# Optimization experiments

Hardware: AMD Instinct MI355X
Metric: run time of the kernel (lower is better)

Reference implementation:

```python
import math
import jax, jax.numpy as jnp
import numpy as np

T = 4096          # sequence length
H = 2048          # hidden_size
I = 8192          # intermediate_size = 4*H
LAYER_ID = 1
N_LAYERS = 24
EPS = 1e-5        # layer_norm_epsilon


def setup_inputs() -> dict:
    key = jax.random.key(0)
    ks = jax.random.split(key, 8)
    s = 1.0 / math.sqrt(H)
    si = 1.0 / math.sqrt(I)
    r0 = LAYER_ID / (N_LAYERS - 1)          # ratio_0_to_1
    r1 = 1.0 - LAYER_ID / N_LAYERS          # ratio_1_to_almost_0
    h = jnp.arange(H, dtype=jnp.float32)
    x = h / H
    time_decay = -5.0 + 8.0 * (h / (H - 1)) ** (0.7 + 1.3 * r0)
    zigzag = 0.5 * ((jnp.arange(1, H + 1) % 3).astype(jnp.float32) - 1.0)
    time_first = jnp.full((H,), math.log(0.3), jnp.float32) + zigzag
    tm_key = x ** r1
    tm_value = tm_key + 0.3 * r0
    tm_recep = x ** (0.5 * r1)
    return {
        "hidden": jax.random.normal(ks[0], (T, H), jnp.float32),
        "att_sx": jnp.zeros((H,), jnp.float32),
        "att_aa": jnp.zeros((H,), jnp.float32),
        "att_bb": jnp.zeros((H,), jnp.float32),
        "att_pp": jnp.full((H,), -1e30, jnp.float32),  # log-space -inf init
        "ffd_sx": jnp.zeros((H,), jnp.float32),
        "ln1_scale": jnp.ones((H,), jnp.float32),
        "ln1_bias": jnp.zeros((H,), jnp.float32),
        "ln2_scale": jnp.ones((H,), jnp.float32),
        "ln2_bias": jnp.zeros((H,), jnp.float32),
        "time_decay": time_decay.astype(jnp.float32),
        "time_first": time_first,
        "tm_key": tm_key.astype(jnp.float32),
        "tm_value": tm_value.astype(jnp.float32),
        "tm_recep": tm_recep.astype(jnp.float32),
        "Wk": jax.random.normal(ks[1], (H, H), jnp.float32) * s,
        "Wv": jax.random.normal(ks[2], (H, H), jnp.float32) * s,
        "Wr": jax.random.normal(ks[3], (H, H), jnp.float32) * s,
        "Wo": jax.random.normal(ks[4], (H, H), jnp.float32) * s,
        "ffn_tm_key": (x ** r1).astype(jnp.float32),
        "ffn_tm_recep": (x ** (0.5 * r1)).astype(jnp.float32),
        "Wfk": jax.random.normal(ks[5], (H, I), jnp.float32) * s,
        "Wfr": jax.random.normal(ks[6], (H, H), jnp.float32) * s,
        "Wfv": jax.random.normal(ks[7], (I, H), jnp.float32) * si,
    }


def _ln(x, scale, bias):
    mu = jnp.mean(x, axis=-1, keepdims=True)
    var = jnp.mean(jnp.square(x - mu), axis=-1, keepdims=True)
    return (x - mu) * jax.lax.rsqrt(var + EPS) * scale + bias


def _block(hidden, att_sx, att_aa, att_bb, att_pp, ffd_sx,
           ln1_scale, ln1_bias, ln2_scale, ln2_bias,
           time_decay, time_first, tm_key, tm_value, tm_recep,
           Wk, Wv, Wr, Wo, ffn_tm_key, ffn_tm_recep, Wfk, Wfr, Wfv):
    # ---- attention (WKV) sub-block ----
    x1 = _ln(hidden, ln1_scale, ln1_bias)               # [T,H]
    c_x = jnp.concatenate((att_sx[None, :], x1[:-1, :]), axis=0)  # token shift
    kx = x1 * tm_key + c_x * (1.0 - tm_key)
    vx = x1 * tm_value + c_x * (1.0 - tm_value)
    rx = x1 * tm_recep + c_x * (1.0 - tm_recep)
    r = jax.nn.sigmoid(rx @ Wr)                         # [T,H]
    k = kx @ Wk
    v = vx @ Wv
    w_decay = -jnp.exp(time_decay)                      # [H]

    def step(carry, kv):
        aa, bb, pp = carry
        kk, vv = kv
        ww = time_first + kk
        p = jnp.maximum(pp, ww)
        e1 = jnp.exp(pp - p)
        e2 = jnp.exp(ww - p)
        out_t = (e1 * aa + e2 * vv) / (e1 * bb + e2)
        ww2 = w_decay + pp
        p2 = jnp.maximum(ww2, kk)
        e1b = jnp.exp(ww2 - p2)
        e2b = jnp.exp(kk - p2)
        return (e1b * aa + e2b * vv, e1b * bb + e2b, p2), out_t

    (aa, bb, pp), cx = jax.lax.scan(step, (att_aa, att_bb, att_pp), (k, v))
    attention = x1 + (r * cx) @ Wo                      # inner residual (as in source)
    hidden2 = hidden + attention

    # ---- feed-forward (channel-mix) sub-block ----
    x2 = _ln(hidden2, ln2_scale, ln2_bias)
    sx2 = jnp.concatenate((ffd_sx[None, :], x2[:-1, :]), axis=0)
    fk = x2 * ffn_tm_key + sx2 * (1.0 - ffn_tm_key)
    fr = x2 * ffn_tm_recep + sx2 * (1.0 - ffn_tm_recep)
    rr = jax.nn.sigmoid(fr @ Wfr)
    kk2 = jnp.square(jax.nn.relu(fk @ Wfk))             # [T,I]
    ffn = rr * (kk2 @ Wfv)
    out = hidden2 + ffn
    return out, x1[-1, :], aa, bb, pp, x2[-1, :]


def reference(hidden, att_sx, att_aa, att_bb, att_pp, ffd_sx,
              ln1_scale, ln1_bias, ln2_scale, ln2_bias,
              time_decay, time_first, tm_key, tm_value, tm_recep,
              Wk, Wv, Wr, Wo, ffn_tm_key, ffn_tm_recep, Wfk, Wfr, Wfv):
    return _block(hidden, att_sx, att_aa, att_bb, att_pp, ffd_sx,
                  ln1_scale, ln1_bias, ln2_scale, ln2_bias,
                  time_decay, time_first, tm_key, tm_value, tm_recep,
                  Wk, Wv, Wr, Wo, ffn_tm_key, ffn_tm_recep, Wfk, Wfr, Wfv)
```

## Files before the change

### kernel.cpp

```cpp
#include <hip/hip_runtime.h>

#define T_SEQ 4096
#define HD 2048
#define ID 8192
#define LN_EPS 1e-5f
#define NCH 64
#define CHL 64
#define CHSZ ((size_t)NCH * HD)

typedef __attribute__((ext_vector_type(4))) float f32x4;
typedef __attribute__((ext_vector_type(8))) short short8;
typedef __attribute__((ext_vector_type(4))) unsigned short ushort4v;

#define GLB(p) ((const __attribute__((address_space(1))) void*)(p))
#define LDSP(p) ((__attribute__((address_space(3))) void*)(p))

__device__ __forceinline__ unsigned short f2bf(float f) {
  union { float f; unsigned int u; } x; x.f = f;
  unsigned int r = x.u + 0x7fffu + ((x.u >> 16) & 1u);
  return (unsigned short)(r >> 16);
}
__device__ __forceinline__ float bf2f(unsigned short u) {
  union { unsigned int i; float f; } x; x.i = ((unsigned int)u) << 16;
  return x.f;
}

__global__ void k_wt(const float* __restrict__ W, unsigned short* __restrict__ Wt,
                     int Nfull, int k_base, int n_base, int Kout) {
  __shared__ float tile[64][65];
  int tx = threadIdx.x, ty = threadIdx.y;
  int n0 = blockIdx.x * 64, k0 = blockIdx.y * 64;
#pragma unroll
  for (int j = 0; j < 8; ++j) {
    int k = ty + 8 * j;
    tile[k][tx] = W[(size_t)(k_base + k0 + k) * Nfull + n_base + n0 + tx];
  }
  __syncthreads();
#pragma unroll
  for (int j = 0; j < 8; ++j) {
    int n = ty + 8 * j;
    Wt[(size_t)(n0 + n) * Kout + k0 + tx] = f2bf(tile[tx][n]);
  }
}

__global__ void k_ln(const float* __restrict__ x, const float* __restrict__ sc,
                     const float* __restrict__ bi, unsigned short* __restrict__ y,
                     float* __restrict__ lastrow) {
  int row = blockIdx.x, tid = threadIdx.x;
  const float* xr = x + (size_t)row * HD;
  f32x4 v0 = *(const f32x4*)(xr + tid * 4);
  f32x4 v1 = *(const f32x4*)(xr + 1024 + tid * 4);
  float s = 0.f, s2 = 0.f;
#pragma unroll
  for (int q = 0; q < 4; ++q) { s += v0[q] + v1[q]; s2 += v0[q] * v0[q] + v1[q] * v1[q]; }
#pragma unroll
  for (int o = 32; o; o >>= 1) { s += __shfl_xor(s, o); s2 += __shfl_xor(s2, o); }
  __shared__ float red[8];
  int wv = tid >> 6;
  if ((tid & 63) == 0) { red[wv] = s; red[4 + wv] = s2; }
  __syncthreads();
  if (tid == 0) {
    float a = red[0] + red[1] + red[2] + red[3];
    float b = red[4] + red[5] + red[6] + red[7];
    float mu = a * (1.f / HD);
    float var = b * (1.f / HD) - mu * mu;
    red[0] = mu; red[1] = rsqrtf(var + LN_EPS);
  }
  __syncthreads();
  float mu = red[0], rs = red[1];
  f32x4 s0 = *(const f32x4*)(sc + tid * 4), s1 = *(const f32x4*)(sc + 1024 + tid * 4);
  f32x4 b0 = *(const f32x4*)(bi + tid * 4), b1 = *(const f32x4*)(bi + 1024 + tid * 4);
  float o0[4], o1[4];
  ushort4v y0, y1;
#pragma unroll
  for (int q = 0; q < 4; ++q) {
    o0[q] = (v0[q] - mu) * rs * s0[q] + b0[q];
    o1[q] = (v1[q] - mu) * rs * s1[q] + b1[q];
    y0[q] = f2bf(o0[q]); y1[q] = f2bf(o1[q]);
  }
  unsigned short* yr = y + (size_t)row * HD;
  *(ushort4v*)(yr + tid * 4) = y0;
  *(ushort4v*)(yr + 1024 + tid * 4) = y1;
  if (row == T_SEQ - 1) {
#pragma unroll
    for (int q = 0; q < 4; ++q) {
      lastrow[tid * 4 + q] = o0[q];
      lastrow[1024 + tid * 4 + q] = o1[q];
    }
  }
}

__global__ void k_mix_att(const unsigned short* __restrict__ x1, const float* __restrict__ sx,
                          const float* __restrict__ tk, const float* __restrict__ tv,
                          const float* __restrict__ tr,
                          unsigned short* __restrict__ kx, unsigned short* __restrict__ vx,
                          unsigned short* __restrict__ rx) {
  size_t idx = ((size_t)blockIdx.x * 256 + threadIdx.x) * 4;
  int h = (int)(idx & (HD - 1));
  ushort4v xu = *(const ushort4v*)(x1 + idx);
  f32x4 x, c;
#pragma unroll
  for (int q = 0; q < 4; ++q) x[q] = bf2f(xu[q]);
  if (idx >= HD) {
    ushort4v cu = *(const ushort4v*)(x1 + idx - HD);
#pragma unroll
    for (int q = 0; q < 4; ++q) c[q] = bf2f(cu[q]);
  } else {
    c = *(const f32x4*)(sx + h);
  }
  f32x4 a = *(const f32x4*)(tk + h);
  f32x4 b = *(const f32x4*)(tv + h);
  f32x4 r = *(const f32x4*)(tr + h);
  ushort4v ok, ov, orr;
#pragma unroll
  for (int q = 0; q < 4; ++q) {
    ok[q] = f2bf(x[q] * a[q] + c[q] * (1.f - a[q]));
    ov[q] = f2bf(x[q] * b[q] + c[q] * (1.f - b[q]));
    orr[q] = f2bf(x[q] * r[q] + c[q] * (1.f - r[q]));
  }
  *(ushort4v*)(kx + idx) = ok;
  *(ushort4v*)(vx + idx) = ov;
  *(ushort4v*)(rx + idx) = orr;
}

__global__ void k_mix_ffn(const unsigned short* __restrict__ x2, const float* __restrict__ sx,
                          const float* __restrict__ tk, const float* __restrict__ tr,
                          unsigned short* __restrict__ fk, unsigned short* __restrict__ fr) {
  size_t idx = ((size_t)blockIdx.x * 256 + threadIdx.x) * 4;
  int h = (int)(idx & (HD - 1));
  ushort4v xu = *(const ushort4v*)(x2 + idx);
  f32x4 x, c;
#pragma unroll
  for (int q = 0; q < 4; ++q) x[q] = bf2f(xu[q]);
  if (idx >= HD) {
    ushort4v cu = *(const ushort4v*)(x2 + idx - HD);
#pragma unroll
    for (int q = 0; q < 4; ++q) c[q] = bf2f(cu[q]);
  } else {
    c = *(const f32x4*)(sx + h);
  }
  f32x4 a = *(const f32x4*)(tk + h);
  f32x4 r = *(const f32x4*)(tr + h);
  ushort4v ok, orr;
#pragma unroll
  for (int q = 0; q < 4; ++q) {
    ok[q] = f2bf(x[q] * a[q] + c[q] * (1.f - a[q]));
    orr[q] = f2bf(x[q] * r[q] + c[q] * (1.f - r[q]));
  }
  *(ushort4v*)(fk + idx) = ok;
  *(ushort4v*)(fr + idx) = orr;
}

__global__ void k_scan1(const unsigned short* __restrict__ kb,
                        const unsigned short* __restrict__ vb,
                        const float* __restrict__ td, float* __restrict__ scr) {
  int c = blockIdx.x >> 3;
  int h = (blockIdx.x & 7) * 256 + threadIdx.x;
  float wd = -__expf(td[h]);
  float a = 0.f, b = 0.f, p = -1e30f;
  size_t base = (size_t)c * CHL * HD + h;
#pragma unroll 4
  for (int u = 0; u < CHL; ++u) {
    float kk = bf2f(kb[base]), vv = bf2f(vb[base]);
    base += HD;
    float ww2 = wd + p;
    float p2 = fmaxf(ww2, kk);
    float e1 = __expf(ww2 - p2), e2 = __expf(kk - p2);
    a = e1 * a + e2 * vv;
    b = e1 * b + e2;
    p = p2;
  }
  size_t i = (size_t)c * HD + h;
  scr[i] = a;
  scr[CHSZ + i] = b;
  scr[2 * CHSZ + i] = p;
}

__global__ void k_scan2(const float* __restrict__ scr, float* __restrict__ stscr,
                        const float* __restrict__ aa0, const float* __restrict__ bb0,
                        const float* __restrict__ pp0, const float* __restrict__ td,
                        float* __restrict__ st) {
  int h = blockIdx.x * 256 + threadIdx.x;
  float aa = aa0[h], bb = bb0[h], pp = pp0[h];
  float wdL = -__expf(td[h]) * (float)CHL;
  for (int c = 0; c < NCH; ++c) {
    size_t i = (size_t)c * HD + h;
    stscr[i] = aa;
    stscr[CHSZ + i] = bb;
    stscr[2 * CHSZ + i] = pp;
    float ca = scr[i], cb = scr[CHSZ + i], cp = scr[2 * CHSZ + i];
    float ww2 = wdL + pp;
    float p2 = fmaxf(ww2, cp);
    float e1 = __expf(ww2 - p2), e2 = __expf(cp - p2);
    aa = e1 * aa + e2 * ca;
    bb = e1 * bb + e2 * cb;
    pp = p2;
  }
  st[HD + h] = aa;
  st[2 * HD + h] = bb;
  st[3 * HD + h] = pp;
}

__global__ void k_scan3(const unsigned short* __restrict__ kb,
                        const unsigned short* __restrict__ vb,
                        const unsigned short* __restrict__ rb,
                        const float* __restrict__ tf_, const float* __restrict__ td,
                        const float* __restrict__ stscr, unsigned short* __restrict__ rcx) {
  int c = blockIdx.x >> 3;
  int h = (blockIdx.x & 7) * 256 + threadIdx.x;
  size_t i0 = (size_t)c * HD + h;
  float aa = stscr[i0], bb = stscr[CHSZ + i0], pp = stscr[2 * CHSZ + i0];
  float tf = tf_[h];
  float wd = -__expf(td[h]);
  size_t base = (size_t)c * CHL * HD + h;
#pragma unroll 4
  for (int u = 0; u < CHL; ++u) {
    float kk = bf2f(kb[base]), vv = bf2f(vb[base]), rv = bf2f(rb[base]);
    float ww = tf + kk;
    float p = fmaxf(pp, ww);
    float e1 = __expf(pp - p), e2 = __expf(ww - p);
    float cx = (e1 * aa + e2 * vv) / (e1 * bb + e2);
    rcx[base] = f2bf(rv * cx);
    float ww2 = wd + pp;
    float p2 = fmaxf(ww2, kk);
    float e1b = __expf(ww2 - p2), e2b = __expf(kk - p2);
    aa = e1b * aa + e2b * vv;
    bb = e1b * bb + e2b;
    pp = p2;
    base += HD;
  }
}

#define MFMA_Q(mh, nh, bset)                                                   \
  _Pragma("unroll") for (int i_ = 0; i_ < 4; ++i_)                             \
  _Pragma("unroll") for (int j_ = 0; j_ < 2; ++j_)                             \
  _Pragma("unroll") for (int ks_ = 0; ks_ < 2; ++ks_)                          \
    acc[(mh)*4 + i_][(nh)*2 + j_] = __builtin_amdgcn_mfma_f32_16x16x32_bf16(   \
        aS[i_ * 2 + ks_], bset[j_ * 2 + ks_], acc[(mh)*4 + i_][(nh)*2 + j_], 0, 0, 0);

#define RD_A(mh)                                                               \
  { const char* pa_ = Ab + arow0 + (mh)*8192;                                  \
    aS[0] = *(const short8*)(pa_ + 0 * 2048 + swz0);                           \
    aS[1] = *(const short8*)(pa_ + 0 * 2048 + swz1);                           \
    aS[2] = *(const short8*)(pa_ + 1 * 2048 + swz0);                           \
    aS[3] = *(const short8*)(pa_ + 1 * 2048 + swz1);                           \
    aS[4] = *(const short8*)(pa_ + 2 * 2048 + swz0);                           \
    aS[5] = *(const short8*)(pa_ + 2 * 2048 + swz1);                           \
    aS[6] = *(const short8*)(pa_ + 3 * 2048 + swz0);                           \
    aS[7] = *(const short8*)(pa_ + 3 * 2048 + swz1); }

#define RD_B(arr, nh)                                                          \
  { const char* pb_ = Bb + brow0 + (nh)*4096;                                  \
    arr[0] = *(const short8*)(pb_ + 0 * 2048 + swz0);                          \
    arr[1] = *(const short8*)(pb_ + 0 * 2048 + swz1);                          \
    arr[2] = *(const short8*)(pb_ + 1 * 2048 + swz0);                          \
    arr[3] = *(const short8*)(pb_ + 1 * 2048 + swz1); }

#define RD_AH(ih)                                                              \
  { const char* pa_ = Ab + arow0 + (ih)*4096;                                  \
    aS[(ih)*4 + 0] = *(const short8*)(pa_ + 0 * 2048 + swz0);                  \
    aS[(ih)*4 + 1] = *(const short8*)(pa_ + 0 * 2048 + swz1);                  \
    aS[(ih)*4 + 2] = *(const short8*)(pa_ + 1 * 2048 + swz0);                  \
    aS[(ih)*4 + 3] = *(const short8*)(pa_ + 1 * 2048 + swz1); }

#define MFMA_H(ih, nh, bset)                                                   \
  _Pragma("unroll") for (int i2_ = 0; i2_ < 2; ++i2_)                          \
  _Pragma("unroll") for (int j_ = 0; j_ < 2; ++j_)                             \
  _Pragma("unroll") for (int ks_ = 0; ks_ < 2; ++ks_)                          \
    acc[(ih)*2 + i2_][(nh)*2 + j_] = __builtin_amdgcn_mfma_f32_16x16x32_bf16(  \
        aS[(ih)*4 + i2_ * 2 + ks_], bset[j_ * 2 + ks_],                        \
        acc[(ih)*2 + i2_][(nh)*2 + j_], 0, 0, 0);

template <int EPI>
__global__ __launch_bounds__(512, 2) void k_gemm256(
    const unsigned short* __restrict__ A, const unsigned short* __restrict__ A1,
    const unsigned short* __restrict__ A2,
    const unsigned short* __restrict__ Bt, const unsigned short* __restrict__ Bt1,
    const unsigned short* __restrict__ Bt2,
    int M, int N, int K, int lda,
    unsigned short* __restrict__ Cb, unsigned short* __restrict__ Cb1,
    unsigned short* __restrict__ Cb2) {
  if (blockIdx.z == 1) { A = A1; Bt = Bt1; Cb = Cb1; }
  else if (blockIdx.z == 2) { A = A2; Bt = Bt2; Cb = Cb2; }
  __shared__ char lds[131072];
  int tid = threadIdx.x;
  int wid = tid >> 6, lane = tid & 63;
  int row_l = lane & 15, kg = lane >> 4;
  int warp_m = wid >> 2, warp_n = wid & 3;
  int m0 = blockIdx.x * 256, n0 = blockIdx.y * 256;

  f32x4 acc[8][4];
#pragma unroll
  for (int i = 0; i < 8; ++i)
#pragma unroll
    for (int j = 0; j < 4; ++j)
#pragma unroll
      for (int q = 0; q < 4; ++q) acc[i][j][q] = 0.f;

  int srow = tid >> 3;
  int schunk = (tid & 7) ^ (srow & 7);
  const unsigned short* Asrc = A + (size_t)(m0 + srow) * lda + schunk * 8;
  const unsigned short* Bsrc = Bt + (size_t)(n0 + srow) * K + schunk * 8;
  char* ldsw = lds + wid * 1024;

  auto STAGE_A = [&](int d, int kt) {
#pragma unroll
    for (int h = 0; h < 2; ++h) {
      const unsigned short* s = Asrc + (size_t)(h * 128) * lda + kt;
      char* dst = ldsw + d * 65536 + h * 16384;
      __builtin_amdgcn_global_load_lds(GLB(s), LDSP(dst), 16, 0, 0);
      __builtin_amdgcn_global_load_lds(GLB(s + (size_t)64 * lda), LDSP(dst + 8192), 16, 0, 0);
    }
  };
  auto STAGE_B = [&](int d, int kt) {
#pragma unroll
    for (int h = 0; h < 2; ++h) {
      const unsigned short* s = Bsrc + (size_t)(h * 128) * K + kt;
      char* dst = ldsw + d * 65536 + 32768 + h * 16384;
      __builtin_amdgcn_global_load_lds(GLB(s), LDSP(dst), 16, 0, 0);
      __builtin_amdgcn_global_load_lds(GLB(s + (size_t)64 * K), LDSP(dst + 8192), 16, 0, 0);
    }
  };

  int swz0 = ((kg) ^ (row_l & 7)) << 4;
  int swz1 = ((4 + kg) ^ (row_l & 7)) << 4;
  int arow0 = (warp_m * 128 + row_l) * 128;
  int brow0 = (warp_n * 64 + row_l) * 128;

  short8 aS[8], b0[4], b1[4];
  int nt = K >> 6;
  STAGE_A(0, 0);
  STAGE_B(0, 0);

#pragma unroll 1
  for (int t = 0; t < nt; ++t) {
    int d = t & 1;
    const char* Ab = lds + d * 65536;
    const char* Bb = lds + d * 65536 + 32768;
    bool pre = (t + 1 < nt);
    int kn = (t + 1) << 6;
    if (pre) {
      STAGE_A(d ^ 1, kn);
      asm volatile("s_waitcnt vmcnt(4)" ::: "memory");
    } else {
      asm volatile("s_waitcnt vmcnt(0)" ::: "memory");
    }
    __builtin_amdgcn_s_barrier();
    RD_A(0)
    RD_B(b0, 0)
    asm volatile("s_waitcnt lgkmcnt(0)" ::: "memory");
    __builtin_amdgcn_s_setprio(1);
    MFMA_Q(0, 0, b0)
    __builtin_amdgcn_s_setprio(0);
    __builtin_amdgcn_s_barrier();
    if (pre) STAGE_B(d ^ 1, kn);
    RD_B(b1, 1)
    asm volatile("s_waitcnt lgkmcnt(0)" ::: "memory");
    __builtin_amdgcn_s_setprio(1);
    MFMA_Q(0, 1, b1)
    __builtin_amdgcn_s_setprio(0);
    __builtin_amdgcn_s_barrier();
    RD_A(1)
    asm volatile("s_waitcnt lgkmcnt(0)" ::: "memory");
    __builtin_amdgcn_s_setprio(1);
    MFMA_Q(1, 1, b1)
    __builtin_amdgcn_s_setprio(0);
    __builtin_amdgcn_s_barrier();
    __builtin_amdgcn_s_setprio(1);
    MFMA_Q(1, 0, b0)
    __builtin_amdgcn_s_setprio(0);
    __builtin_amdgcn_s_barrier();
  }

#pragma unroll
  for (int i = 0; i < 8; ++i) {
#pragma unroll
    for (int j = 0; j < 4; ++j) {
#pragma unroll
      for (int q = 0; q < 4; ++q) {
        int r = m0 + warp_m * 128 + i * 16 + kg * 4 + q;
        int c = n0 + warp_n * 64 + j * 16 + row_l;
        size_t idx = (size_t)r * N + c;
        float val = acc[i][j][q];
        if (EPI == 2) { float t2 = val > 0.f ? val * val : 0.f; Cb[idx] = f2bf(t2); }
        if (EPI == 8) {
          float o = (blockIdx.z == 2) ? 1.f / (1.f + __expf(-val)) : val;
          Cb[idx] = f2bf(o);
        }
      }
    }
  }
}

template <int EPI>
__global__ __launch_bounds__(512) void k_gemmB(
    const unsigned short* __restrict__ A, const unsigned short* __restrict__ Bt,
    int M, int N, int K, int lda, float* __restrict__ C,
    unsigned short* __restrict__ Cb, const float* __restrict__ E0,
    const unsigned short* __restrict__ E1b, const unsigned short* __restrict__ E0b) {
  __shared__ char lds[147456];
  int tid = threadIdx.x;
  int wid = tid >> 6, lane = tid & 63;
  int row_l = lane & 15, kg = lane >> 4;
  int warp_m = wid >> 2, warp_n = wid & 3;
  int m0 = blockIdx.x * 128, n0 = blockIdx.y * 256;

  f32x4 acc[4][4];
#pragma unroll
  for (int i = 0; i < 4; ++i)
#pragma unroll
    for (int j = 0; j < 4; ++j)
#pragma unroll
      for (int q = 0; q < 4; ++q) acc[i][j][q] = 0.f;

  int srow = tid >> 3;
  int schunk = (tid & 7) ^ (srow & 7);
  const unsigned short* Asrc = A + (size_t)(m0 + srow) * lda + schunk * 8;
  const unsigned short* Bsrc = Bt + (size_t)(n0 + srow) * K + schunk * 8;
  int wsw = wid * 1024;

  auto STAGE_P1 = [&](int d, int kt) {
    char* base = lds + d * 49152;
    __builtin_amdgcn_global_load_lds(GLB(Asrc + kt), LDSP(base + wsw), 16, 0, 0);
    __builtin_amdgcn_global_load_lds(GLB(Asrc + (size_t)64 * lda + kt),
                                     LDSP(base + 8192 + wsw), 16, 0, 0);
    __builtin_amdgcn_global_load_lds(GLB(Bsrc + kt), LDSP(base + 16384 + wsw), 16, 0, 0);
  };
  auto STAGE_P2 = [&](int d, int kt) {
    char* base = lds + d * 49152;
#pragma unroll
    for (int h = 1; h < 4; ++h)
      __builtin_amdgcn_global_load_lds(GLB(Bsrc + (size_t)(h * 64) * K + kt),
                                       LDSP(base + 16384 + h * 8192 + wsw), 16, 0, 0);
  };

  int swz0 = ((kg) ^ (row_l & 7)) << 4;
  int swz1 = ((4 + kg) ^ (row_l & 7)) << 4;
  int arow0 = (warp_m * 64 + row_l) * 128;
  int brow0 = (warp_n * 64 + row_l) * 128;

  short8 aS[8], b0[4], b1[4];
  int nt = K >> 6;
  STAGE_P1(0, 0); STAGE_P2(0, 0);
  STAGE_P1(1, 64); STAGE_P2(1, 64);

#pragma unroll 1
  for (int t = 0; t < nt; ++t) {
    int d = t % 3;
    const char* Ab = lds + d * 49152;
    const char* Bb = lds + d * 49152 + 16384;
    int b2 = t + 2 < nt ? (t + 2) % 3 : 0;
    int k2 = (t + 2) << 6;
    if (t + 2 < nt) {
      STAGE_P1(b2, k2);
      asm volatile("s_waitcnt vmcnt(9)" ::: "memory");
    } else if (t + 1 < nt) {
      asm volatile("s_waitcnt vmcnt(6)" ::: "memory");
    } else {
      asm volatile("s_waitcnt vmcnt(0)" ::: "memory");
    }
    __builtin_amdgcn_s_barrier();
    RD_AH(0)
    RD_B(b0, 0)
    asm volatile("s_waitcnt lgkmcnt(0)" ::: "memory");
    __builtin_amdgcn_s_setprio(1);
    MFMA_H(0, 0, b0)
    __builtin_amdgcn_s_setprio(0);
    __builtin_amdgcn_s_barrier();
    if (t + 2 < nt) STAGE_P2(b2, k2);
    RD_AH(1)
    asm volatile("s_waitcnt lgkmcnt(0)" ::: "memory");
    __builtin_amdgcn_s_setprio(1);
    MFMA_H(1, 0, b0)
    __builtin_amdgcn_s_setprio(0);
    __builtin_amdgcn_s_barrier();
    RD_B(b1, 1)
    asm volatile("s_waitcnt lgkmcnt(0)" ::: "memory");
    __builtin_amdgcn_s_setprio(1);
    MFMA_H(0, 1, b1)
    __builtin_amdgcn_s_setprio(0);
    __builtin_amdgcn_s_barrier();
    __builtin_amdgcn_s_setprio(1);
    MFMA_H(1, 1, b1)
    __builtin_amdgcn_s_setprio(0);
    __builtin_amdgcn_s_barrier();
  }

#pragma unroll
  for (int i = 0; i < 4; ++i) {
#pragma unroll
    for (int j = 0; j < 4; ++j) {
#pragma unroll
      for (int q = 0; q < 4; ++q) {
        int r = m0 + warp_m * 64 + i * 16 + kg * 4 + q;
        int c = n0 + warp_n * 64 + j * 16 + row_l;
        size_t idx = (size_t)r * N + c;
        float val = acc[i][j][q];
        if (EPI == 3) C[idx] = val + E0[idx] + bf2f(E1b[idx]);
        if (EPI == 6) Cb[idx] = f2bf(1.f / (1.f + __expf(-val)));
        if (EPI == 7) C[idx] += bf2f(E0b[idx]) * val;
      }
    }
  }
}

extern "C" void kernel_launch(void* const* d_in, const int* in_sizes, int n_in,
                              void* d_out, int out_size, void* d_ws, size_t ws_size,
                              hipStream_t stream) {
  (void)in_sizes; (void)n_in; (void)out_size; (void)ws_size;
  const float* hidden     = (const float*)d_in[0];
  const float* att_sx     = (const float*)d_in[1];
  const float* att_aa     = (const float*)d_in[2];
  const float* att_bb     = (const float*)d_in[3];
  const float* att_pp     = (const float*)d_in[4];
  const float* ffd_sx     = (const float*)d_in[5];
  const float* ln1_s      = (const float*)d_in[6];
  const float* ln1_b      = (const float*)d_in[7];
  const float* ln2_s      = (const float*)d_in[8];
  const float* ln2_b      = (const float*)d_in[9];
  const float* time_decay = (const float*)d_in[10];
  const float* time_first = (const float*)d_in[11];
  const float* tm_key     = (const float*)d_in[12];
  const float* tm_value   = (const float*)d_in[13];
  const float* tm_recep   = (const float*)d_in[14];
  const float* Wk         = (const float*)d_in[15];
  const float* Wv         = (const float*)d_in[16];
  const float* Wr         = (const float*)d_in[17];
  const float* Wo         = (const float*)d_in[18];
  const float* ffn_tm_key = (const float*)d_in[19];
  const float* ffn_tm_rec = (const float*)d_in[20];
  const float* Wfk        = (const float*)d_in[21];
  const float* Wfr        = (const float*)d_in[22];
  const float* Wfv        = (const float*)d_in[23];
  float* out = (float*)d_out;
  float* st = out + (size_t)T_SEQ * HD;

  const size_t MB8 = (size_t)HD * HD * 2;
  const size_t PG = (size_t)T_SEQ * HD * 2;
  char* w = (char*)d_ws;
  unsigned short* s0 = (unsigned short*)(w);
  unsigned short* s1 = (unsigned short*)(w + MB8);
  unsigned short* s2 = (unsigned short*)(w + 2 * MB8);
  unsigned short* s3 = (unsigned short*)(w + 3 * MB8);
  char* pA = w + 4 * MB8;
  char* pB = pA + PG;
  char* pC = pB + PG;
  char* pD = pC + PG;
  char* pE = pD + PG;
  char* pF = pE + PG;

  unsigned short* kx   = (unsigned short*)pA;
  unsigned short* vx   = (unsigned short*)pB;
  unsigned short* rx   = (unsigned short*)pC;
  unsigned short* kbf  = (unsigned short*)pD;
  unsigned short* x1bf = (unsigned short*)pE;
  unsigned short* vbf  = (unsigned short*)pF;
  unsigned short* rbf  = (unsigned short*)out;
  unsigned short* rcx  = (unsigned short*)pC;
  unsigned short* x2bf = (unsigned short*)pD;
  unsigned short* fk   = (unsigned short*)pF;
  unsigned short* fr   = (unsigned short*)pB;
  unsigned short* rr   = (unsigned short*)pA;
  unsigned short* kk2  = (unsigned short*)pB;
  float* scr   = (float*)s0;
  float* stscr = (float*)s1;

  dim3 tb64(64, 8);
  dim3 wg64(HD / 64, HD / 64);
  dim3 gB(T_SEQ / 128, HD / 256);

  k_wt<<<wg64, tb64, 0, stream>>>(Wk, s0, HD, 0, 0, HD);
  k_wt<<<wg64, tb64, 0, stream>>>(Wv, s1, HD, 0, 0, HD);
  k_wt<<<wg64, tb64, 0, stream>>>(Wr, s2, HD, 0, 0, HD);
  k_wt<<<wg64, tb64, 0, stream>>>(Wo, s3, HD, 0, 0, HD);
  k_ln<<<T_SEQ, 256, 0, stream>>>(hidden, ln1_s, ln1_b, x1bf, st);
  k_mix_att<<<T_SEQ * HD / 1024, 256, 0, stream>>>(x1bf, att_sx, tm_key, tm_value, tm_recep,
                                                   kx, vx, rx);
  k_gemm256<8><<<dim3(T_SEQ / 256, HD / 256, 3), 512, 0, stream>>>(
      kx, vx, rx, s0, s1, s2, T_SEQ, HD, HD, HD, kbf, vbf, rbf);
  k_scan1<<<NCH * 8, 256, 0, stream>>>(kbf, vbf, time_decay, scr);
  k_scan2<<<HD / 256, 256, 0, stream>>>(scr, stscr, att_aa, att_bb, att_pp, time_decay, st);
  k_scan3<<<NCH * 8, 256, 0, stream>>>(kbf, vbf, rbf, time_first, time_decay, stscr, rcx);
  k_gemmB<3><<<gB, 512, 0, stream>>>(rcx, s3, T_SEQ, HD, HD, HD, out, nullptr,
                                     hidden, x1bf, nullptr);

  k_ln<<<T_SEQ, 256, 0, stream>>>(out, ln2_s, ln2_b, x2bf, st + 4 * HD);
  k_mix_ffn<<<T_SEQ * HD / 1024, 256, 0, stream>>>(x2bf, ffd_sx, ffn_tm_key, ffn_tm_rec,
                                                   fk, fr);
  k_wt<<<wg64, tb64, 0, stream>>>(Wfr, s3, HD, 0, 0, HD);
  k_gemmB<6><<<gB, 512, 0, stream>>>(fr, s3, T_SEQ, HD, HD, HD, nullptr, rr,
                                     nullptr, nullptr, nullptr);
  for (int q = 0; q < 4; ++q)
    k_wt<<<wg64, tb64, 0, stream>>>(Wfk, s0 + (size_t)q * 2048 * 2048, ID, 0, q * 2048, HD);
  k_gemm256<2><<<dim3(T_SEQ / 256, ID / 256), 512, 0, stream>>>(
      fk, nullptr, nullptr, s0, nullptr, nullptr, T_SEQ, ID, HD, HD,
      kk2, nullptr, nullptr);
  for (int q = 0; q < 4; ++q)
    k_wt<<<dim3(HD / 64, HD / 64), tb64, 0, stream>>>(Wfv, s0 + (size_t)q * 2048, HD,
                                                      q * 2048, 0, ID);
  k_gemmB<7><<<gB, 512, 0, stream>>>(kk2, s0, T_SEQ, HD, ID, ID, out, nullptr,
                                     nullptr, nullptr, rr);
}
```

Measured before the change: 643.3 us.

## Load B operand directly from global into registers in k_gemmB, shrink LDS

```diff
diff --git a/kernel.cpp b/kernel.cpp
--- a/kernel.cpp
+++ b/kernel.cpp
@@ -268,7 +268,7 @@
   _Pragma("unroll") for (int j_ = 0; j_ < 2; ++j_)                             \
   _Pragma("unroll") for (int ks_ = 0; ks_ < 2; ++ks_)                          \
     acc[(ih)*2 + i2_][(nh)*2 + j_] = __builtin_amdgcn_mfma_f32_16x16x32_bf16(  \
-        aS[(ih)*4 + i2_ * 2 + ks_], bset[j_ * 2 + ks_],                        \
+        aS[(ih)*4 + i2_ * 2 + ks_], (bset)[j_ * 2 + ks_],                      \
         acc[(ih)*2 + i2_][(nh)*2 + j_], 0, 0, 0);
 
 template <int EPI>
@@ -398,7 +398,7 @@
     int M, int N, int K, int lda, float* __restrict__ C,
     unsigned short* __restrict__ Cb, const float* __restrict__ E0,
     const unsigned short* __restrict__ E1b, const unsigned short* __restrict__ E0b) {
-  __shared__ char lds[147456];
+  __shared__ char lds[32768];
   int tid = threadIdx.x;
   int wid = tid >> 6, lane = tid & 63;
   int row_l = lane & 15, kg = lane >> 4;
@@ -416,74 +416,60 @@
   int srow = tid >> 3;
   int schunk = (tid & 7) ^ (srow & 7);
   const unsigned short* Asrc = A + (size_t)(m0 + srow) * lda + schunk * 8;
-  const unsigned short* Bsrc = Bt + (size_t)(n0 + srow) * K + schunk * 8;
   int wsw = wid * 1024;
-
-  auto STAGE_P1 = [&](int d, int kt) {
-    char* base = lds + d * 49152;
+  const unsigned short* Bg = Bt + (size_t)(n0 + warp_n * 64 + row_l) * K + kg * 8;
+
+  auto STAGE_A = [&](int d, int kt) {
+    char* base = lds + d * 16384;
     __builtin_amdgcn_global_load_lds(GLB(Asrc + kt), LDSP(base + wsw), 16, 0, 0);
     __builtin_amdgcn_global_load_lds(GLB(Asrc + (size_t)64 * lda + kt),
                                      LDSP(base + 8192 + wsw), 16, 0, 0);
-    __builtin_amdgcn_global_load_lds(GLB(Bsrc + kt), LDSP(base + 16384 + wsw), 16, 0, 0);
   };
-  auto STAGE_P2 = [&](int d, int kt) {
-    char* base = lds + d * 49152;
-#pragma unroll
-    for (int h = 1; h < 4; ++h)
-      __builtin_amdgcn_global_load_lds(GLB(Bsrc + (size_t)(h * 64) * K + kt),
-                                       LDSP(base + 16384 + h * 8192 + wsw), 16, 0, 0);
-  };
+
+#define LOADB_(arr, kt)                                                        \
+  _Pragma("unroll") for (int nh_ = 0; nh_ < 2; ++nh_)                          \
+  _Pragma("unroll") for (int j_ = 0; j_ < 2; ++j_)                             \
+  _Pragma("unroll") for (int ks_ = 0; ks_ < 2; ++ks_)                          \
+    arr[nh_ * 4 + j_ * 2 + ks_] = *(const short8*)(                            \
+        Bg + (size_t)(nh_ * 32 + j_ * 16) * K + ks_ * 32 + (kt));
 
   int swz0 = ((kg) ^ (row_l & 7)) << 4;
   int swz1 = ((4 + kg) ^ (row_l & 7)) << 4;
   int arow0 = (warp_m * 64 + row_l) * 128;
-  int brow0 = (warp_n * 64 + row_l) * 128;
-
-  short8 aS[8], b0[4], b1[4];
+
+  short8 aS[8], bA[8], bB[8];
   int nt = K >> 6;
-  STAGE_P1(0, 0); STAGE_P2(0, 0);
-  STAGE_P1(1, 64); STAGE_P2(1, 64);
+  STAGE_A(0, 0);
+  LOADB_(bA, 0)
+
+#define BODY_(t, bc, bn)                                                       \
+  {                                                                            \
+    const char* Ab = lds + ((t) & 1) * 16384;                                  \
+    if ((t) + 1 < nt) {                                                        \
+      int kn_ = ((t) + 1) << 6;                                                \
+      STAGE_A(((t) & 1) ^ 1, kn_);                                             \
+      LOADB_(bn, kn_)                                                          \
+      asm volatile("s_waitcnt vmcnt(10)" ::: "memory");                        \
+    } else {                                                                   \
+      asm volatile("s_waitcnt vmcnt(0)" ::: "memory");                         \
+    }                                                                          \
+    __builtin_amdgcn_s_barrier();                                              \
+    RD_AH(0)                                                                   \
+    RD_AH(1)                                                                   \
+    asm volatile("s_waitcnt lgkmcnt(0)" ::: "memory");                         \
+    __builtin_amdgcn_s_setprio(1);                                             \
+    MFMA_H(0, 0, bc)                                                           \
+    MFMA_H(1, 0, bc)                                                           \
+    MFMA_H(0, 1, (bc) + 4)                                                     \
+    MFMA_H(1, 1, (bc) + 4)                                                     \
+    __builtin_amdgcn_s_setprio(0);                                             \
+    __builtin_amdgcn_s_barrier();                                              \
+  }
 
 #pragma unroll 1
-  for (int t = 0; t < nt; ++t) {
-    int d = t % 3;
-    const char* Ab = lds + d * 49152;
-    const char* Bb = lds + d * 49152 + 16384;
-    int b2 = t + 2 < nt ? (t + 2) % 3 : 0;
-    int k2 = (t + 2) << 6;
-    if (t + 2 < nt) {
-      STAGE_P1(b2, k2);
-      asm volatile("s_waitcnt vmcnt(9)" ::: "memory");
-    } else if (t + 1 < nt) {
-      asm volatile("s_waitcnt vmcnt(6)" ::: "memory");
-    } else {
-      asm volatile("s_waitcnt vmcnt(0)" ::: "memory");
-    }
-    __builtin_amdgcn_s_barrier();
-    RD_AH(0)
-    RD_B(b0, 0)
-    asm volatile("s_waitcnt lgkmcnt(0)" ::: "memory");
-    __builtin_amdgcn_s_setprio(1);
-    MFMA_H(0, 0, b0)
-    __builtin_amdgcn_s_setprio(0);
-    __builtin_amdgcn_s_barrier();
-    if (t + 2 < nt) STAGE_P2(b2, k2);
-    RD_AH(1)
-    asm volatile("s_waitcnt lgkmcnt(0)" ::: "memory");
-    __builtin_amdgcn_s_setprio(1);
-    MFMA_H(1, 0, b0)
-    __builtin_amdgcn_s_setprio(0);
-    __builtin_amdgcn_s_barrier();
-    RD_B(b1, 1)
-    asm volatile("s_waitcnt lgkmcnt(0)" ::: "memory");
-    __builtin_amdgcn_s_setprio(1);
-    MFMA_H(0, 1, b1)
-    __builtin_amdgcn_s_setprio(0);
-    __builtin_amdgcn_s_barrier();
-    __builtin_amdgcn_s_setprio(1);
-    MFMA_H(1, 1, b1)
-    __builtin_amdgcn_s_setprio(0);
-    __builtin_amdgcn_s_barrier();
+  for (int t = 0; t < nt; t += 2) {
+    BODY_(t, bA, bB)
+    BODY_(t + 1, bB, bA)
   }
 
 #pragma unroll
```

New measurement: 868.1 us. 35.0% more time.

## Use split-K 256x256 GEMM with atomic epilogue for FFN down-projection

Applied to the files above, without the earlier changes.

```diff
diff --git a/kernel.cpp b/kernel.cpp
--- a/kernel.cpp
+++ b/kernel.cpp
@@ -268,7 +268,7 @@
   _Pragma("unroll") for (int j_ = 0; j_ < 2; ++j_)                             \
   _Pragma("unroll") for (int ks_ = 0; ks_ < 2; ++ks_)                          \
     acc[(ih)*2 + i2_][(nh)*2 + j_] = __builtin_amdgcn_mfma_f32_16x16x32_bf16(  \
-        aS[(ih)*4 + i2_ * 2 + ks_], bset[j_ * 2 + ks_],                        \
+        aS[(ih)*4 + i2_ * 2 + ks_], (bset)[j_ * 2 + ks_],                      \
         acc[(ih)*2 + i2_][(nh)*2 + j_], 0, 0, 0);
 
 template <int EPI>
@@ -277,11 +277,17 @@
     const unsigned short* __restrict__ A2,
     const unsigned short* __restrict__ Bt, const unsigned short* __restrict__ Bt1,
     const unsigned short* __restrict__ Bt2,
-    int M, int N, int K, int lda,
+    int M, int N, int K, int lda, int ldb,
     unsigned short* __restrict__ Cb, unsigned short* __restrict__ Cb1,
-    unsigned short* __restrict__ Cb2) {
-  if (blockIdx.z == 1) { A = A1; Bt = Bt1; Cb = Cb1; }
-  else if (blockIdx.z == 2) { A = A2; Bt = Bt2; Cb = Cb2; }
+    unsigned short* __restrict__ Cb2, float* __restrict__ C,
+    const unsigned short* __restrict__ E0b) {
+  int koff = 0;
+  if (EPI == 9) {
+    koff = blockIdx.z * K;
+  } else {
+    if (blockIdx.z == 1) { A = A1; Bt = Bt1; Cb = Cb1; }
+    else if (blockIdx.z == 2) { A = A2; Bt = Bt2; Cb = Cb2; }
+  }
   __shared__ char lds[131072];
   int tid = threadIdx.x;
   int wid = tid >> 6, lane = tid & 63;
@@ -299,8 +305,8 @@
 
   int srow = tid >> 3;
   int schunk = (tid & 7) ^ (srow & 7);
-  const unsigned short* Asrc = A + (size_t)(m0 + srow) * lda + schunk * 8;
-  const unsigned short* Bsrc = Bt + (size_t)(n0 + srow) * K + schunk * 8;
+  const unsigned short* Asrc = A + (size_t)(m0 + srow) * lda + koff + schunk * 8;
+  const unsigned short* Bsrc = Bt + (size_t)(n0 + srow) * ldb + koff + schunk * 8;
   char* ldsw = lds + wid * 1024;
 
   auto STAGE_A = [&](int d, int kt) {
@@ -315,10 +321,10 @@
   auto STAGE_B = [&](int d, int kt) {
 #pragma unroll
     for (int h = 0; h < 2; ++h) {
-      const unsigned short* s = Bsrc + (size_t)(h * 128) * K + kt;
+      const unsigned short* s = Bsrc + (size_t)(h * 128) * ldb + kt;
       char* dst = ldsw + d * 65536 + 32768 + h * 16384;
       __builtin_amdgcn_global_load_lds(GLB(s), LDSP(dst), 16, 0, 0);
-      __builtin_amdgcn_global_load_lds(GLB(s + (size_t)64 * K), LDSP(dst + 8192), 16, 0, 0);
+      __builtin_amdgcn_global_load_lds(GLB(s + (size_t)64 * ldb), LDSP(dst + 8192), 16, 0, 0);
     }
   };
 
@@ -387,6 +393,7 @@
           float o = (blockIdx.z == 2) ? 1.f / (1.f + __expf(-val)) : val;
           Cb[idx] = f2bf(o);
         }
+        if (EPI == 9) unsafeAtomicAdd(&C[idx], bf2f(E0b[idx]) * val);
       }
     }
   }
@@ -577,7 +584,7 @@
   k_mix_att<<<T_SEQ * HD / 1024, 256, 0, stream>>>(x1bf, att_sx, tm_key, tm_value, tm_recep,
                                                    kx, vx, rx);
   k_gemm256<8><<<dim3(T_SEQ / 256, HD / 256, 3), 512, 0, stream>>>(
-      kx, vx, rx, s0, s1, s2, T_SEQ, HD, HD, HD, kbf, vbf, rbf);
+      kx, vx, rx, s0, s1, s2, T_SEQ, HD, HD, HD, HD, kbf, vbf, rbf, nullptr, nullptr);
   k_scan1<<<NCH * 8, 256, 0, stream>>>(kbf, vbf, time_decay, scr);
   k_scan2<<<HD / 256, 256, 0, stream>>>(scr, stscr, att_aa, att_bb, att_pp, time_decay, st);
   k_scan3<<<NCH * 8, 256, 0, stream>>>(kbf, vbf, rbf, time_first, time_decay, stscr, rcx);
@@ -593,11 +600,12 @@
   for (int q = 0; q < 4; ++q)
     k_wt<<<wg64, tb64, 0, stream>>>(Wfk, s0 + (size_t)q * 2048 * 2048, ID, 0, q * 2048, HD);
   k_gemm256<2><<<dim3(T_SEQ / 256, ID / 256), 512, 0, stream>>>(
-      fk, nullptr, nullptr, s0, nullptr, nullptr, T_SEQ, ID, HD, HD,
-      kk2, nullptr, nullptr);
+      fk, nullptr, nullptr, s0, nullptr, nullptr, T_SEQ, ID, HD, HD, HD,
+      kk2, nullptr, nullptr, nullptr, nullptr);
   for (int q = 0; q < 4; ++q)
     k_wt<<<dim3(HD / 64, HD / 64), tb64, 0, stream>>>(Wfv, s0 + (size_t)q * 2048, HD,
                                                       q * 2048, 0, ID);
-  k_gemmB<7><<<gB, 512, 0, stream>>>(kk2, s0, T_SEQ, HD, ID, ID, out, nullptr,
-                                     nullptr, nullptr, rr);
-}
+  k_gemm256<9><<<dim3(T_SEQ / 256, HD / 256, 2), 512, 0, stream>>>(
+      kk2, nullptr, nullptr, s0, nullptr, nullptr, T_SEQ, HD, ID / 2, ID, ID,
+      nullptr, nullptr, nullptr, out, rr);
+}
```

After: 665.8 us. 3.5% more time.
